# Optimization experiments

Hardware: AMD Instinct MI355X
Metric: run time of the kernel (lower is better)

Reference implementation:

```python
import jax, jax.numpy as jnp
import numpy as np

N = 16384   # total nodes
M = 512     # molecules
D_IN = 64
D_OUT = 64
NEG = -1e9  # mask value for nodes outside a molecule


def setup_inputs() -> dict:
    key = jax.random.key(0)
    ks = jax.random.split(key, 8)
    node_features = jax.random.normal(ks[0], (N, D_IN), dtype=jnp.float32)
    e = jax.random.uniform(ks[1], (N, N), dtype=jnp.float32) * (2.0 / N)
    # molecule membership: sorted segment ids -> one-hot membership matrix
    seg = np.sort(np.asarray(jax.random.randint(ks[2], (N,), 0, M)))
    mnm = (seg[None, :] == np.arange(M)[:, None]).astype(np.float32)
    mol_node_matrix = jnp.asarray(mnm)
    mol_node_mask = jnp.asarray((1.0 - mnm) * NEG)
    s = 1.0 / np.sqrt(D_IN)
    W0 = jax.random.uniform(ks[3], (D_OUT, D_IN), jnp.float32, -s, s)
    b0 = jnp.zeros((D_OUT,), jnp.float32)
    W1 = jax.random.uniform(ks[4], (D_OUT, D_OUT), jnp.float32, -s, s)
    b1 = jnp.zeros((D_OUT,), jnp.float32)
    w2 = jax.random.uniform(ks[5], (1, D_OUT), jnp.float32, -s, s)
    b2 = jnp.zeros((1,), jnp.float32)
    return dict(node_features=node_features, e=e,
                mol_node_matrix=mol_node_matrix, mol_node_mask=mol_node_mask,
                W0=W0, b0=b0, W1=W1, b1=b1, w2=w2, b2=b2)


def reference(node_features, e, mol_node_matrix, mol_node_mask, W0, b0, W1, b1, w2, b2):
    # GraphConvolutionLayer: two linears with adjacency matmul, LeakyReLU between
    h = e @ (node_features @ W0.T + b0)            # [N, D_OUT]
    h = jax.nn.leaky_relu(h, negative_slope=0.01)
    h = e @ (h @ W1.T + b1)                        # [N, D_OUT]
    h = jnp.tanh(h)
    # attention logits per node; mol_node_matrix @ diag(a) == mnm * a^T (broadcast)
    a = (h @ w2.T + b2).reshape(-1)                # [N]
    logits = mol_node_matrix * a[None, :] + mol_node_mask  # [M, N]
    mol_node_weight = jax.nn.softmax(logits, axis=1)
    return mol_node_weight @ h, mol_node_weight
```

## Files before the change

### kernel.cpp

```cpp
#include <hip/hip_runtime.h>
#include <hip/hip_bf16.h>

#define NN 16384
#define MM 512
#define DD 64
#define BK 128
#define BM 32
#define ITERS (NN / BK)
#define BK2 256
#define ITERS2 (NN / BK2)

typedef __attribute__((ext_vector_type(8))) short short8;
typedef __attribute__((ext_vector_type(4))) float f32x4;
typedef __attribute__((ext_vector_type(4))) short short4v;
typedef __attribute__((ext_vector_type(4))) unsigned u32x4;

#define SE 2097152.0f
#define INV_SE 4.76837158203125e-07f

__device__ __forceinline__ short f2bf(float f) {
  union { __hip_bfloat16 b; short s; } u;
  u.b = __float2bfloat16(f);
  return u.s;
}

__device__ __forceinline__ short8 cvt8(f32x4 a, f32x4 b) {
  short8 r;
  r[0] = f2bf(a[0]); r[1] = f2bf(a[1]); r[2] = f2bf(a[2]); r[3] = f2bf(a[3]);
  r[4] = f2bf(b[0]); r[5] = f2bf(b[1]); r[6] = f2bf(b[2]); r[7] = f2bf(b[3]);
  return r;
}

typedef __attribute__((address_space(1))) const unsigned gu32;
typedef __attribute__((address_space(3))) unsigned lu32;
__device__ __forceinline__ void gld16(const void* g, void* l) {
  __builtin_amdgcn_global_load_lds((gu32*)g, (lu32*)l, 16, 0, 0);
}

template <int OFMT>
__global__ __launch_bounds__(256) void linear_mfma(const float* __restrict__ in,
                                                   const float* __restrict__ W,
                                                   const float* __restrict__ b,
                                                   void* __restrict__ xt_) {
  const int t = threadIdx.x, lane = t & 63, w = t >> 6;
  const int rl = lane & 15, hi = lane >> 4;
  const int r0 = blockIdx.x * 64 + w * 16;
  const float* ap = in + (size_t)(r0 + rl) * DD + hi * 8;

  f32x4 acc[4];
#pragma unroll
  for (int g = 0; g < 4; ++g) {
    const float bias = b[g * 16 + rl];
    acc[g][0] = bias; acc[g][1] = bias; acc[g][2] = bias; acc[g][3] = bias;
  }
#pragma unroll
  for (int kk = 0; kk < DD; kk += 32) {
    const short8 af = cvt8(*(const f32x4*)(ap + kk), *(const f32x4*)(ap + kk + 4));
#pragma unroll
    for (int g = 0; g < 4; ++g) {
      const float* wp = W + (size_t)(g * 16 + rl) * DD + hi * 8 + kk;
      const short8 wf = cvt8(*(const f32x4*)wp, *(const f32x4*)(wp + 4));
      acc[g] = __builtin_amdgcn_mfma_f32_16x16x32_bf16(af, wf, acc[g], 0, 0, 0);
    }
  }
#pragma unroll
  for (int g = 0; g < 4; ++g) {
    if (OFMT == 0) {
      unsigned short* xt = (unsigned short*)xt_;
      short4v s;
      s[0] = f2bf(acc[g][0]); s[1] = f2bf(acc[g][1]);
      s[2] = f2bf(acc[g][2]); s[3] = f2bf(acc[g][3]);
      *(short4v*)(xt + (size_t)(g * 16 + rl) * NN + r0 + hi * 4) = s;
    } else {
      unsigned char* xt = (unsigned char*)xt_;
      int pk = __builtin_amdgcn_cvt_pk_fp8_f32(acc[g][0], acc[g][1], 0, false);
      pk = __builtin_amdgcn_cvt_pk_fp8_f32(acc[g][2], acc[g][3], pk, true);
      *(unsigned*)(xt + (size_t)(g * 16 + rl) * NN + r0 + hi * 4) = (unsigned)pk;
    }
  }
}

__global__ __launch_bounds__(256) void gemm1(const float* __restrict__ e,
                                             const unsigned short* __restrict__ xt,
                                             float* __restrict__ out,
                                             unsigned char* __restrict__ e8) {
  __shared__ float Ab[2][BM * BK];
  __shared__ unsigned short Bb[2][64 * BK];
  const int t = threadIdx.x, lane = t & 63, w = t >> 6;
  const int rl = lane & 15, hi = lane >> 4;
  const int wr = w >> 1, wc = w & 1;
  const int r0 = blockIdx.x * BM;
  const int it0 = (blockIdx.x * 37) & (ITERS - 1);

  auto STAGE = [&](int buf, int it) {
    const int k0 = ((it0 + it) & (ITERS - 1)) * BK;
#pragma unroll
    for (int j = 0; j < 4; ++j) {
      const int row = w * 8 + j * 2 + (lane >> 5);
      const float* src =
          e + (size_t)(r0 + row) * NN + k0 + (((lane & 31) ^ (row & 7)) << 2);
      gld16(src, &Ab[buf][(w * 8 + j * 2) * BK]);
    }
#pragma unroll
    for (int j = 0; j < 4; ++j) {
      const int col = w * 16 + j * 4 + (lane >> 4);
      const unsigned short* src =
          xt + (size_t)col * NN + k0 + (((lane & 15) ^ (col & 7)) << 3);
      gld16(src, &Bb[buf][(w * 16 + j * 4) * BK]);
    }
  };

  f32x4 acc[2];
  acc[0][0] = acc[0][1] = acc[0][2] = acc[0][3] = 0.f;
  acc[1][0] = acc[1][1] = acc[1][2] = acc[1][3] = 0.f;

  STAGE(0, 0);
#pragma unroll 1
  for (int it = 0; it < ITERS; ++it) {
    const int cur = it & 1;
    const int k0c = ((it0 + it) & (ITERS - 1)) * BK;
    if (it + 1 < ITERS) {
      STAGE(cur ^ 1, it + 1);
      asm volatile("s_waitcnt vmcnt(8)" ::: "memory");
    } else {
      asm volatile("s_waitcnt vmcnt(0)" ::: "memory");
    }
    __builtin_amdgcn_s_barrier();
    asm volatile("" ::: "memory");
    {
      const int r = t >> 3, j0 = t & 7;
      const float* arw = &Ab[cur][r * BK];
      u32x4 dw;
#pragma unroll
      for (int i = 0; i < 4; ++i) {
        const int c = j0 * 4 + i;
        f32x4 q = *(const f32x4*)&arw[(c ^ (r & 7)) << 2];
        int d2 = __builtin_amdgcn_cvt_pk_fp8_f32(q[0] * SE, q[1] * SE, 0, false);
        d2 = __builtin_amdgcn_cvt_pk_fp8_f32(q[2] * SE, q[3] * SE, d2, true);
        dw[i] = (unsigned)d2;
      }
      *(u32x4*)(e8 + (size_t)(r0 + r) * NN + k0c + j0 * 16) = dw;
    }
#pragma unroll
    for (int kk = 0; kk < BK; kk += 32) {
      const int ca = (kk >> 2) + hi * 2;
      const int arow = (wr * 16 + rl) * BK;
      f32x4 a0 = *(const f32x4*)&Ab[cur][arow + ((ca ^ (rl & 7)) << 2)];
      f32x4 a1 = *(const f32x4*)&Ab[cur][arow + (((ca + 1) ^ (rl & 7)) << 2)];
      const short8 af = cvt8(a0, a1);
      const int cb = (kk >> 3) + hi;
#pragma unroll
      for (int g = 0; g < 2; ++g) {
        const int col = wc * 32 + g * 16 + rl;
        const short8 bf =
            *(const short8*)&Bb[cur][col * BK + ((cb ^ (rl & 7)) << 3)];
        acc[g] = __builtin_amdgcn_mfma_f32_16x16x32_bf16(af, bf, acc[g], 0, 0, 0);
      }
    }
    asm volatile("" ::: "memory");
    __builtin_amdgcn_s_barrier();
  }

#pragma unroll
  for (int g = 0; g < 2; ++g) {
    const int col = wc * 32 + g * 16 + rl;
#pragma unroll
    for (int j = 0; j < 4; ++j) {
      float v = acc[g][j];
      v = (v > 0.f) ? v : 0.01f * v;
      out[(size_t)(r0 + wr * 16 + hi * 4 + j) * DD + col] = v;
    }
  }
}

__global__ __launch_bounds__(256) void gemm2_fp8(const unsigned char* __restrict__ e8,
                                                 const unsigned char* __restrict__ xt8,
                                                 const float* __restrict__ w2,
                                                 const float* __restrict__ b2,
                                                 float* __restrict__ out,
                                                 float* __restrict__ av) {
  __shared__ unsigned char Ab2[2][BM * BK2];
  __shared__ unsigned char Bb2[2][64 * BK2];
  __shared__ float aacc[2][16];
  const int t = threadIdx.x, lane = t & 63, w = t >> 6;
  const int rl = lane & 15, hi = lane >> 4;
  const int wr = w >> 1, wc = w & 1;
  const int r0 = blockIdx.x * BM;
  const int it0 = (blockIdx.x * 37) & (ITERS2 - 1);

  auto STAGE = [&](int buf, int it) {
    const int k0 = ((it0 + it) & (ITERS2 - 1)) * BK2;
#pragma unroll
    for (int j = 0; j < 2; ++j) {
      const int row = w * 8 + j * 4 + (lane >> 4);
      const unsigned char* src =
          e8 + (size_t)(r0 + row) * NN + k0 + (((lane & 15) ^ (row & 15)) << 4);
      gld16(src, &Ab2[buf][(w * 8 + j * 4) * BK2]);
    }
#pragma unroll
    for (int j = 0; j < 4; ++j) {
      const int col = w * 16 + j * 4 + (lane >> 4);
      const unsigned char* src =
          xt8 + (size_t)col * NN + k0 + (((lane & 15) ^ (col & 15)) << 4);
      gld16(src, &Bb2[buf][(w * 16 + j * 4) * BK2]);
    }
  };

  f32x4 acc[2];
  acc[0][0] = acc[0][1] = acc[0][2] = acc[0][3] = 0.f;
  acc[1][0] = acc[1][1] = acc[1][2] = acc[1][3] = 0.f;

  STAGE(0, 0);
#pragma unroll 1
  for (int it = 0; it < ITERS2; ++it) {
    const int cur = it & 1;
    if (it + 1 < ITERS2) {
      STAGE(cur ^ 1, it + 1);
      asm volatile("s_waitcnt vmcnt(6)" ::: "memory");
    } else {
      asm volatile("s_waitcnt vmcnt(0)" ::: "memory");
    }
    __builtin_amdgcn_s_barrier();
    asm volatile("" ::: "memory");
    const unsigned char* arw = &Ab2[cur][(wr * 16 + rl) * BK2];
#pragma unroll
    for (int kk = 0; kk < BK2; kk += 32) {
      const int ca = (kk >> 4) + (hi >> 1);
      const int off = (hi & 1) * 8;
      const long af = *(const long*)&arw[((ca ^ (rl & 15)) << 4) + off];
#pragma unroll
      for (int g = 0; g < 2; ++g) {
        const int col = wc * 32 + g * 16 + rl;
        const long bf =
            *(const long*)&Bb2[cur][col * BK2 + ((ca ^ (col & 15)) << 4) + off];
        acc[g] = __builtin_amdgcn_mfma_f32_16x16x32_fp8_fp8(af, bf, acc[g], 0, 0, 0);
      }
    }
    asm volatile("" ::: "memory");
    __builtin_amdgcn_s_barrier();
  }

  float hv[2][4];
#pragma unroll
  for (int g = 0; g < 2; ++g) {
    const int col = wc * 32 + g * 16 + rl;
#pragma unroll
    for (int j = 0; j < 4; ++j) {
      hv[g][j] = tanhf(acc[g][j] * INV_SE);
      out[(size_t)(r0 + wr * 16 + hi * 4 + j) * DD + col] = hv[g][j];
    }
  }
  const float w2a = w2[wc * 32 + rl], w2b = w2[wc * 32 + 16 + rl];
  float rp[4];
#pragma unroll
  for (int j = 0; j < 4; ++j) rp[j] = hv[0][j] * w2a + hv[1][j] * w2b;
#pragma unroll
  for (int off = 1; off < 16; off <<= 1)
#pragma unroll
    for (int j = 0; j < 4; ++j) rp[j] += __shfl_xor(rp[j], off);
  if (wc == 0 && rl == 0) {
#pragma unroll
    for (int j = 0; j < 4; ++j) aacc[wr][hi * 4 + j] = rp[j];
  }
  __syncthreads();
  if (wc == 1 && rl == 0) {
    const float bb = b2[0];
#pragma unroll
    for (int j = 0; j < 4; ++j)
      av[r0 + wr * 16 + hi * 4 + j] = aacc[wr][hi * 4 + j] + rp[j] + bb;
  }
}

__global__ __launch_bounds__(256) void softmax_pool(const float* __restrict__ mnm,
                                                    const float* __restrict__ a,
                                                    const float* __restrict__ h,
                                                    float* __restrict__ wout,
                                                    float* __restrict__ out0) {
  __shared__ float red[256];
  __shared__ int redi[256];
  __shared__ float partial[4][64];
  const int m = blockIdx.x, t = threadIdx.x;
  const size_t base = (size_t)m * NN;
  const f32x4* mnm4 = (const f32x4*)(mnm + base);
  const f32x4* a4 = (const f32x4*)a;
  f32x4* wout4 = (f32x4*)(wout + base);

  f32x4 lg[16];
  float mx = -3.0e38f;
  int mn_n = NN, mx_n = -1;
#pragma unroll
  for (int i = 0; i < 16; ++i) {
    const int idx = t + i * 256;
    const f32x4 mv = mnm4[idx];
    const f32x4 av = a4[idx];
    f32x4 v;
#pragma unroll
    for (int j = 0; j < 4; ++j) {
      const bool mem = mv[j] > 0.5f;
      v[j] = mem ? av[j] : -3.0e38f;
      if (mem) {
        const int n = idx * 4 + j;
        mn_n = min(mn_n, n);
        mx_n = max(mx_n, n);
      }
    }
    lg[i] = v;
    mx = fmaxf(mx, fmaxf(fmaxf(v[0], v[1]), fmaxf(v[2], v[3])));
  }
  red[t] = mx; redi[t] = mn_n; __syncthreads();
  for (int s = 128; s > 0; s >>= 1) {
    if (t < s) {
      red[t] = fmaxf(red[t], red[t + s]);
      redi[t] = min(redi[t], redi[t + s]);
    }
    __syncthreads();
  }
  mx = red[0];
  const int ns = redi[0];
  __syncthreads();
  redi[t] = mx_n; __syncthreads();
  for (int s = 128; s > 0; s >>= 1) {
    if (t < s) redi[t] = max(redi[t], redi[t + s]);
    __syncthreads();
  }
  const int ne = redi[0];
  __syncthreads();

  const bool empty = (ne < 0);
  float sm = 0.f;
#pragma unroll
  for (int i = 0; i < 16; ++i) {
    f32x4 v = lg[i];
#pragma unroll
    for (int j = 0; j < 4; ++j)
      v[j] = empty ? 1.0f : ((v[j] > -1.0e38f) ? expf(v[j] - mx) : 0.0f);
    lg[i] = v;
    sm += v[0] + v[1] + v[2] + v[3];
  }
  red[t] = sm; __syncthreads();
  for (int s = 128; s > 0; s >>= 1) {
    if (t < s) red[t] += red[t + s];
    __syncthreads();
  }
  const float inv = 1.0f / red[0];
#pragma unroll
  for (int i = 0; i < 16; ++i) wout4[t + i * 256] = lg[i] * inv;

  __threadfence_block();
  __syncthreads();

  const int s0 = empty ? 0 : ns;
  const int e0 = empty ? NN : ne + 1;
  const int d = t & 63, sub = t >> 6;
  const float* wrow = wout + base;
  float accp = 0.f;
  for (int n = s0 + sub; n < e0; n += 4)
    accp += wrow[n] * h[(size_t)n * DD + d];
  partial[sub][d] = accp;
  __syncthreads();
  if (t < 64)
    out0[m * DD + t] =
        partial[0][t] + partial[1][t] + partial[2][t] + partial[3][t];
}

extern "C" void kernel_launch(void* const* d_in, const int* in_sizes, int n_in,
                              void* d_out, int out_size, void* d_ws, size_t ws_size,
                              hipStream_t stream) {
  const float* nf  = (const float*)d_in[0];
  const float* e   = (const float*)d_in[1];
  const float* mnm = (const float*)d_in[2];
  const float* W0  = (const float*)d_in[4];
  const float* b0  = (const float*)d_in[5];
  const float* W1  = (const float*)d_in[6];
  const float* b1  = (const float*)d_in[7];
  const float* w2  = (const float*)d_in[8];
  const float* b2  = (const float*)d_in[9];

  char* ws = (char*)d_ws;
  unsigned short* XT0 = (unsigned short*)(ws);
  unsigned char*  XT8 = (unsigned char*)(ws + (size_t)2 * 1024 * 1024);
  float* h1 = (float*)(ws + (size_t)4 * 1024 * 1024);
  float* h  = (float*)(ws + (size_t)8 * 1024 * 1024);
  float* av = (float*)(ws + (size_t)12 * 1024 * 1024);
  unsigned char* e8 = (unsigned char*)(ws + (size_t)16 * 1024 * 1024);

  float* out0 = (float*)d_out;
  float* wout = out0 + (size_t)MM * DD;

  linear_mfma<0><<<256, 256, 0, stream>>>(nf, W0, b0, XT0);
  gemm1<<<512, 256, 0, stream>>>(e, XT0, h1, e8);
  linear_mfma<1><<<256, 256, 0, stream>>>(h1, W1, b1, XT8);
  gemm2_fp8<<<512, 256, 0, stream>>>(e8, XT8, w2, b2, h, av);
  softmax_pool<<<512, 256, 0, stream>>>(mnm, av, h, wout, out0);
}
```

Measured before the change: 379.8 us.

## Quantize adjacency to fp8 up front and run both adjacency GEMMs in fp8

Replaces the fused bf16 first GEMM, which also emitted the fp8 copy of e, with a standalone streaming quantize kernel followed by two instances of the fp8 GEMM template. The first GEMM now reads the 1-byte e8 and fp8 features scaled by 32 instead of fp32 e with bf16 features, and the output is rescaled by 2^-26. The full fp32 e read still happens once in the quantize pass, but the first GEMM's work becomes fp8 MFMA with lighter LDS traffic. The cost is an extra kernel launch, more precision loss in the first layer, and possible fp8 range problems for the first-layer features.

```diff
diff --git a/kernel.cpp b/kernel.cpp
--- a/kernel.cpp
+++ b/kernel.cpp
@@ -4,19 +4,22 @@
 #define NN 16384
 #define MM 512
 #define DD 64
-#define BK 128
 #define BM 32
-#define ITERS (NN / BK)
 #define BK2 256
 #define ITERS2 (NN / BK2)
 
 typedef __attribute__((ext_vector_type(8))) short short8;
 typedef __attribute__((ext_vector_type(4))) float f32x4;
-typedef __attribute__((ext_vector_type(4))) short short4v;
-typedef __attribute__((ext_vector_type(4))) unsigned u32x4;
 
 #define SE 2097152.0f
-#define INV_SE 4.76837158203125e-07f
+#define SXF 32.0f
+#define INV26 1.4901161193847656e-08f
+
+typedef __attribute__((address_space(1))) const unsigned gu32;
+typedef __attribute__((address_space(3))) unsigned lu32;
+__device__ __forceinline__ void gld16(const void* g, void* l) {
+  __builtin_amdgcn_global_load_lds((gu32*)g, (lu32*)l, 16, 0, 0);
+}
 
 __device__ __forceinline__ short f2bf(float f) {
   union { __hip_bfloat16 b; short s; } u;
@@ -31,17 +34,22 @@
   return r;
 }
 
-typedef __attribute__((address_space(1))) const unsigned gu32;
-typedef __attribute__((address_space(3))) unsigned lu32;
-__device__ __forceinline__ void gld16(const void* g, void* l) {
-  __builtin_amdgcn_global_load_lds((gu32*)g, (lu32*)l, 16, 0, 0);
-}
-
-template <int OFMT>
-__global__ __launch_bounds__(256) void linear_mfma(const float* __restrict__ in,
-                                                   const float* __restrict__ W,
-                                                   const float* __restrict__ b,
-                                                   void* __restrict__ xt_) {
+__global__ __launch_bounds__(256) void quantize_e(const f32x4* __restrict__ e4,
+                                                  unsigned* __restrict__ e8) {
+  size_t i = (size_t)blockIdx.x * 256 + threadIdx.x;
+#pragma unroll 4
+  for (int it = 0; it < 128; ++it, i += 524288) {
+    f32x4 v = e4[i];
+    int d = __builtin_amdgcn_cvt_pk_fp8_f32(v[0] * SE, v[1] * SE, 0, false);
+    d = __builtin_amdgcn_cvt_pk_fp8_f32(v[2] * SE, v[3] * SE, d, true);
+    e8[i] = (unsigned)d;
+  }
+}
+
+__global__ __launch_bounds__(256) void linear_fp8(const float* __restrict__ in,
+                                                  const float* __restrict__ W,
+                                                  const float* __restrict__ b,
+                                                  unsigned char* __restrict__ xt) {
   const int t = threadIdx.x, lane = t & 63, w = t >> 6;
   const int rl = lane & 15, hi = lane >> 4;
   const int r0 = blockIdx.x * 64 + w * 16;
@@ -65,120 +73,19 @@
   }
 #pragma unroll
   for (int g = 0; g < 4; ++g) {
-    if (OFMT == 0) {
-      unsigned short* xt = (unsigned short*)xt_;
-      short4v s;
-      s[0] = f2bf(acc[g][0]); s[1] = f2bf(acc[g][1]);
-      s[2] = f2bf(acc[g][2]); s[3] = f2bf(acc[g][3]);
-      *(short4v*)(xt + (size_t)(g * 16 + rl) * NN + r0 + hi * 4) = s;
-    } else {
-      unsigned char* xt = (unsigned char*)xt_;
-      int pk = __builtin_amdgcn_cvt_pk_fp8_f32(acc[g][0], acc[g][1], 0, false);
-      pk = __builtin_amdgcn_cvt_pk_fp8_f32(acc[g][2], acc[g][3], pk, true);
-      *(unsigned*)(xt + (size_t)(g * 16 + rl) * NN + r0 + hi * 4) = (unsigned)pk;
-    }
-  }
-}
-
-__global__ __launch_bounds__(256) void gemm1(const float* __restrict__ e,
-                                             const unsigned short* __restrict__ xt,
-                                             float* __restrict__ out,
-                                             unsigned char* __restrict__ e8) {
-  __shared__ float Ab[2][BM * BK];
-  __shared__ unsigned short Bb[2][64 * BK];
-  const int t = threadIdx.x, lane = t & 63, w = t >> 6;
-  const int rl = lane & 15, hi = lane >> 4;
-  const int wr = w >> 1, wc = w & 1;
-  const int r0 = blockIdx.x * BM;
-  const int it0 = (blockIdx.x * 37) & (ITERS - 1);
-
-  auto STAGE = [&](int buf, int it) {
-    const int k0 = ((it0 + it) & (ITERS - 1)) * BK;
-#pragma unroll
-    for (int j = 0; j < 4; ++j) {
-      const int row = w * 8 + j * 2 + (lane >> 5);
-      const float* src =
-          e + (size_t)(r0 + row) * NN + k0 + (((lane & 31) ^ (row & 7)) << 2);
-      gld16(src, &Ab[buf][(w * 8 + j * 2) * BK]);
-    }
-#pragma unroll
-    for (int j = 0; j < 4; ++j) {
-      const int col = w * 16 + j * 4 + (lane >> 4);
-      const unsigned short* src =
-          xt + (size_t)col * NN + k0 + (((lane & 15) ^ (col & 7)) << 3);
-      gld16(src, &Bb[buf][(w * 16 + j * 4) * BK]);
-    }
-  };
-
-  f32x4 acc[2];
-  acc[0][0] = acc[0][1] = acc[0][2] = acc[0][3] = 0.f;
-  acc[1][0] = acc[1][1] = acc[1][2] = acc[1][3] = 0.f;
-
-  STAGE(0, 0);
-#pragma unroll 1
-  for (int it = 0; it < ITERS; ++it) {
-    const int cur = it & 1;
-    const int k0c = ((it0 + it) & (ITERS - 1)) * BK;
-    if (it + 1 < ITERS) {
-      STAGE(cur ^ 1, it + 1);
-      asm volatile("s_waitcnt vmcnt(8)" ::: "memory");
-    } else {
-      asm volatile("s_waitcnt vmcnt(0)" ::: "memory");
-    }
-    __builtin_amdgcn_s_barrier();
-    asm volatile("" ::: "memory");
-    {
-      const int r = t >> 3, j0 = t & 7;
-      const float* arw = &Ab[cur][r * BK];
-      u32x4 dw;
-#pragma unroll
-      for (int i = 0; i < 4; ++i) {
-        const int c = j0 * 4 + i;
-        f32x4 q = *(const f32x4*)&arw[(c ^ (r & 7)) << 2];
-        int d2 = __builtin_amdgcn_cvt_pk_fp8_f32(q[0] * SE, q[1] * SE, 0, false);
-        d2 = __builtin_amdgcn_cvt_pk_fp8_f32(q[2] * SE, q[3] * SE, d2, true);
-        dw[i] = (unsigned)d2;
-      }
-      *(u32x4*)(e8 + (size_t)(r0 + r) * NN + k0c + j0 * 16) = dw;
-    }
-#pragma unroll
-    for (int kk = 0; kk < BK; kk += 32) {
-      const int ca = (kk >> 2) + hi * 2;
-      const int arow = (wr * 16 + rl) * BK;
-      f32x4 a0 = *(const f32x4*)&Ab[cur][arow + ((ca ^ (rl & 7)) << 2)];
-      f32x4 a1 = *(const f32x4*)&Ab[cur][arow + (((ca + 1) ^ (rl & 7)) << 2)];
-      const short8 af = cvt8(a0, a1);
-      const int cb = (kk >> 3) + hi;
-#pragma unroll
-      for (int g = 0; g < 2; ++g) {
-        const int col = wc * 32 + g * 16 + rl;
-        const short8 bf =
-            *(const short8*)&Bb[cur][col * BK + ((cb ^ (rl & 7)) << 3)];
-        acc[g] = __builtin_amdgcn_mfma_f32_16x16x32_bf16(af, bf, acc[g], 0, 0, 0);
-      }
-    }
-    asm volatile("" ::: "memory");
-    __builtin_amdgcn_s_barrier();
-  }
-
-#pragma unroll
-  for (int g = 0; g < 2; ++g) {
-    const int col = wc * 32 + g * 16 + rl;
-#pragma unroll
-    for (int j = 0; j < 4; ++j) {
-      float v = acc[g][j];
-      v = (v > 0.f) ? v : 0.01f * v;
-      out[(size_t)(r0 + wr * 16 + hi * 4 + j) * DD + col] = v;
-    }
-  }
-}
-
-__global__ __launch_bounds__(256) void gemm2_fp8(const unsigned char* __restrict__ e8,
-                                                 const unsigned char* __restrict__ xt8,
-                                                 const float* __restrict__ w2,
-                                                 const float* __restrict__ b2,
-                                                 float* __restrict__ out,
-                                                 float* __restrict__ av) {
+    int pk = __builtin_amdgcn_cvt_pk_fp8_f32(acc[g][0] * SXF, acc[g][1] * SXF, 0, false);
+    pk = __builtin_amdgcn_cvt_pk_fp8_f32(acc[g][2] * SXF, acc[g][3] * SXF, pk, true);
+    *(unsigned*)(xt + (size_t)(g * 16 + rl) * NN + r0 + hi * 4) = (unsigned)pk;
+  }
+}
+
+template <int ACT>
+__global__ __launch_bounds__(256) void gemm_fp8(const unsigned char* __restrict__ e8,
+                                                const unsigned char* __restrict__ xt8,
+                                                const float* __restrict__ w2,
+                                                const float* __restrict__ b2,
+                                                float* __restrict__ out,
+                                                float* __restrict__ av) {
   __shared__ unsigned char Ab2[2][BM * BK2];
   __shared__ unsigned char Bb2[2][64 * BK2];
   __shared__ float aacc[2][16];
@@ -246,28 +153,33 @@
     const int col = wc * 32 + g * 16 + rl;
 #pragma unroll
     for (int j = 0; j < 4; ++j) {
-      hv[g][j] = tanhf(acc[g][j] * INV_SE);
-      out[(size_t)(r0 + wr * 16 + hi * 4 + j) * DD + col] = hv[g][j];
-    }
-  }
-  const float w2a = w2[wc * 32 + rl], w2b = w2[wc * 32 + 16 + rl];
-  float rp[4];
-#pragma unroll
-  for (int j = 0; j < 4; ++j) rp[j] = hv[0][j] * w2a + hv[1][j] * w2b;
-#pragma unroll
-  for (int off = 1; off < 16; off <<= 1)
-#pragma unroll
-    for (int j = 0; j < 4; ++j) rp[j] += __shfl_xor(rp[j], off);
-  if (wc == 0 && rl == 0) {
-#pragma unroll
-    for (int j = 0; j < 4; ++j) aacc[wr][hi * 4 + j] = rp[j];
-  }
-  __syncthreads();
-  if (wc == 1 && rl == 0) {
-    const float bb = b2[0];
-#pragma unroll
-    for (int j = 0; j < 4; ++j)
-      av[r0 + wr * 16 + hi * 4 + j] = aacc[wr][hi * 4 + j] + rp[j] + bb;
+      float v = acc[g][j] * INV26;
+      if (ACT == 0) v = (v > 0.f) ? v : 0.01f * v;
+      else v = tanhf(v);
+      hv[g][j] = v;
+      out[(size_t)(r0 + wr * 16 + hi * 4 + j) * DD + col] = v;
+    }
+  }
+  if (ACT == 1) {
+    const float w2a = w2[wc * 32 + rl], w2b = w2[wc * 32 + 16 + rl];
+    float rp[4];
+#pragma unroll
+    for (int j = 0; j < 4; ++j) rp[j] = hv[0][j] * w2a + hv[1][j] * w2b;
+#pragma unroll
+    for (int off = 1; off < 16; off <<= 1)
+#pragma unroll
+      for (int j = 0; j < 4; ++j) rp[j] += __shfl_xor(rp[j], off);
+    if (wc == 0 && rl == 0) {
+#pragma unroll
+      for (int j = 0; j < 4; ++j) aacc[wr][hi * 4 + j] = rp[j];
+    }
+    __syncthreads();
+    if (wc == 1 && rl == 0) {
+      const float bb = b2[0];
+#pragma unroll
+      for (int j = 0; j < 4; ++j)
+        av[r0 + wr * 16 + hi * 4 + j] = aacc[wr][hi * 4 + j] + rp[j] + bb;
+    }
   }
 }
 
@@ -377,8 +289,8 @@
   const float* b2  = (const float*)d_in[9];
 
   char* ws = (char*)d_ws;
-  unsigned short* XT0 = (unsigned short*)(ws);
-  unsigned char*  XT8 = (unsigned char*)(ws + (size_t)2 * 1024 * 1024);
+  unsigned char* XT8_0 = (unsigned char*)(ws);
+  unsigned char* XT8_1 = (unsigned char*)(ws + (size_t)2 * 1024 * 1024);
   float* h1 = (float*)(ws + (size_t)4 * 1024 * 1024);
   float* h  = (float*)(ws + (size_t)8 * 1024 * 1024);
   float* av = (float*)(ws + (size_t)12 * 1024 * 1024);
@@ -387,9 +299,10 @@
   float* out0 = (float*)d_out;
   float* wout = out0 + (size_t)MM * DD;
 
-  linear_mfma<0><<<256, 256, 0, stream>>>(nf, W0, b0, XT0);
-  gemm1<<<512, 256, 0, stream>>>(e, XT0, h1, e8);
-  linear_mfma<1><<<256, 256, 0, stream>>>(h1, W1, b1, XT8);
-  gemm2_fp8<<<512, 256, 0, stream>>>(e8, XT8, w2, b2, h, av);
+  quantize_e<<<2048, 256, 0, stream>>>((const f32x4*)e, (unsigned*)e8);
+  linear_fp8<<<256, 256, 0, stream>>>(nf, W0, b0, XT8_0);
+  gemm_fp8<0><<<512, 256, 0, stream>>>(e8, XT8_0, nullptr, nullptr, h1, nullptr);
+  linear_fp8<<<256, 256, 0, stream>>>(h1, W1, b1, XT8_1);
+  gemm_fp8<1><<<512, 256, 0, stream>>>(e8, XT8_1, w2, b2, h, av);
   softmax_pool<<<512, 256, 0, stream>>>(mnm, av, h, wout, out0);
 }
```

Result: slower. 475.7 us (+25.3%).
